# Optimization experiments

Measured on AMD Instinct MI355X. Metric: run time of the kernel, lower is better.

The kernel has to match this reference:

```python
import jax, jax.numpy as jnp
import numpy as np

BATCH = 4096        # config['batch_size']
N_PARTS = 4         # config['n_parts']
TEMP = 0.1          # config['temp_fac']
D = 256             # embedding dim
BS = 3 * BATCH      # bs = 3 * batch_size
EPS = 1e-6          # CosineSimilarity eps


def setup_inputs() -> dict:
    key = jax.random.key(0)
    reg_pred = jax.random.normal(key, (BS, D), dtype=jnp.float32)
    return {"reg_pred": reg_pred}


def reference(reg_pred):
    B, bs, t = BATCH, BS, TEMP
    # cosine similarity: x/max(||x||, eps)
    nrm = jnp.linalg.norm(reg_pred, axis=1, keepdims=True)
    xn = reg_pred / jnp.maximum(nrm, EPS)
    E = jnp.exp((xn @ xn.T) / t)                      # exp(cos_sim/temp), [bs, bs]

    # negative-index mask: for anchor row a (pos_index p = a % B),
    # excluded indices are range(rem, bs, 4) with rem = p % n_parts
    k = jnp.arange(bs)
    rem = (k % B) % N_PARTS                           # rem per anchor row, [bs]
    excluded = (k[None, :] >= rem[:, None]) & (((k[None, :] - rem[:, None]) % 4) == 0)
    den = jnp.sum(jnp.where(excluded, 0.0, E), axis=1)  # [bs], sum exp(den sims)

    p = jnp.arange(B)
    i1, i2, i3 = p, B + p, 2 * B + p

    def pair_loss(a, b, n):
        # symmetrical NT-Xent-style term; n = exp(num_sim / t)
        return -jnp.log(n / (n + den[a])) - jnp.log(n / (n + den[b]))

    n12 = E[i1, i2]
    n13 = E[i1, i3]
    n23 = E[i2, i3]
    total = jnp.sum(pair_loss(i1, i2, n12)
                    + pair_loss(i1, i3, n13)
                    + pair_loss(i2, i3, n23))
    return total / (2 * B)
```

## Files before the change

### kernel.cpp

```cpp
#include <hip/hip_runtime.h>
#include <hip/hip_bf16.h>
#include <cstdint>
#include <cstddef>

#define BS_TOT 12288
#define DIM    256
#define BATCH_ 4096
#define NTILE  96
#define NPAIR  4656

typedef float f32x16 __attribute__((ext_vector_type(16)));
typedef int   i32x8  __attribute__((ext_vector_type(8)));

__global__ __launch_bounds__(256) void normalize_kernel(const float* __restrict__ x,
                                                        uint8_t* __restrict__ xn,
                                                        float* __restrict__ invn,
                                                        float* __restrict__ den,
                                                        float* __restrict__ out,
                                                        int osz) {
  if (blockIdx.x == 0 && (int)threadIdx.x < osz) out[threadIdx.x] = 0.0f;
  const int wave = threadIdx.x >> 6;
  const int lane = threadIdx.x & 63;
  const int row  = blockIdx.x * 4 + wave;
  const float4 v = ((const float4*)(x + (size_t)row * DIM))[lane];
  float ss = v.x*v.x + v.y*v.y + v.z*v.z + v.w*v.w;
  #pragma unroll
  for (int off = 1; off < 64; off <<= 1) ss += __shfl_xor(ss, off, 64);
  const float s = 1.0f / fmaxf(sqrtf(ss), 1e-6f);
  if (lane == 0) { invn[row] = s; den[row] = 0.0f; }
  const float sc = s * 3.79828286f;
  unsigned int w = __builtin_amdgcn_cvt_pk_fp8_f32(v.x * sc, v.y * sc, 0u, false);
  w = __builtin_amdgcn_cvt_pk_fp8_f32(v.z * sc, v.w * sc, w, true);
  ((unsigned int*)(xn + (size_t)row * DIM))[lane] = w;
}

__global__ __launch_bounds__(512, 4) void gemm_den_kernel(const uint8_t* __restrict__ xn,
                                                          float* __restrict__ den) {
  __shared__ __align__(16) uint8_t As[128 * 256];
  __shared__ __align__(16) uint8_t Bs[128 * 256];

  const int tid = threadIdx.x;

  const int t = blockIdx.x;
  int j = (int)((sqrtf(8.0f * (float)t + 1.0f) - 1.0f) * 0.5f);
  while ((j + 1) * (j + 2) / 2 <= t) j++;
  while (j * (j + 1) / 2 > t) j--;
  const int tI = t - j * (j + 1) / 2;
  const int tJ = j;
  const bool offd = (tI != tJ);

  const int wave = tid >> 6, lane = tid & 63;
  const int wr   = wave >> 2;
  const int wc   = wave & 3;
  const int l31  = lane & 31, half = lane >> 5;

  const uint8_t* Ab = xn + (size_t)tI * 128 * DIM;
  const uint8_t* Bb = xn + (size_t)tJ * 128 * DIM;

  int4 chA[4], chB[4];
  #pragma unroll
  for (int c = 0; c < 4; c++) {
    const int q = c * 512 + tid;
    const size_t off = (size_t)(q >> 4) * DIM + (size_t)(q & 15) * 16;
    chA[c] = *(const int4*)(Ab + off);
    chB[c] = *(const int4*)(Bb + off);
  }
  #pragma unroll
  for (int c = 0; c < 4; c++) {
    const int q   = c * 512 + tid;
    const int row = q >> 4, k16 = q & 15;
    const int wa  = row * 256 + (((k16 >> 1) ^ (row & 7)) * 32) + (k16 & 1) * 16;
    *(int4*)(As + wa) = chA[c];
    *(int4*)(Bs + wa) = chB[c];
  }
  __syncthreads();

  const int e7 = l31 & 7;
  const int rowA0 = (wr * 64 + l31) * 256;
  const int rowB0 = (wc * 32 + l31) * 256;

  f32x16 acc[2]  = {};
  f32x16 accT[2] = {};
  #pragma unroll
  for (int ks = 0; ks < 4; ks++) {
    const int u = ((2 * ks + half) ^ e7) * 32;
    i32x8 af[2], bf;
    af[0] = *(const i32x8*)(As + rowA0 + u);
    af[1] = *(const i32x8*)(As + rowA0 + 32 * 256 + u);
    bf    = *(const i32x8*)(Bs + rowB0 + u);
    #pragma unroll
    for (int mi = 0; mi < 2; mi++)
      acc[mi] = __builtin_amdgcn_mfma_scale_f32_32x32x64_f8f6f4(
          af[mi], bf, acc[mi], 0, 0, 0, 0x7F7F7F7F, 0, 0x7F7F7F7F);
    if (offd) {
      #pragma unroll
      for (int mi = 0; mi < 2; mi++)
        accT[mi] = __builtin_amdgcn_mfma_scale_f32_32x32x64_f8f6f4(
            bf, af[mi], accT[mi], 0, 0, 0, 0x7F7F7F7F, 0, 0x7F7F7F7F);
    }
  }

  {
    float cs = 0.0f;
    #pragma unroll
    for (int mi = 0; mi < 2; mi++)
      #pragma unroll
      for (int r = 0; r < 16; r++)
        if (((l31 ^ r) & 3) != 0)
          cs += __builtin_amdgcn_exp2f(acc[mi][r]);
    cs += __shfl_xor(cs, 32, 64);
    if (half == 0) atomicAdd(&den[tJ * 128 + wc * 32 + l31], cs);
  }
  if (offd) {
    #pragma unroll
    for (int mi = 0; mi < 2; mi++) {
      float cs = 0.0f;
      #pragma unroll
      for (int r = 0; r < 16; r++)
        if (((l31 ^ r) & 3) != 0)
          cs += __builtin_amdgcn_exp2f(accT[mi][r]);
      cs += __shfl_xor(cs, 32, 64);
      if (half == 0) atomicAdd(&den[tI * 128 + wr * 64 + mi * 32 + l31], cs);
    }
  }
}

__global__ __launch_bounds__(256) void loss_kernel(const float* __restrict__ x,
                                                   const float* __restrict__ invn,
                                                   const float* __restrict__ den,
                                                   float* __restrict__ out) {
  __shared__ float part[4];
  const int wave = threadIdx.x >> 6, lane = threadIdx.x & 63;
  const int p = blockIdx.x * 4 + wave;
  const float4 a = ((const float4*)(x + (size_t)p * DIM))[lane];
  const float4 b = ((const float4*)(x + (size_t)(BATCH_ + p) * DIM))[lane];
  const float4 c = ((const float4*)(x + (size_t)(2*BATCH_ + p) * DIM))[lane];
  float d12 = a.x*b.x + a.y*b.y + a.z*b.z + a.w*b.w;
  float d13 = a.x*c.x + a.y*c.y + a.z*c.z + a.w*c.w;
  float d23 = b.x*c.x + b.y*c.y + b.z*c.z + b.w*c.w;
  #pragma unroll
  for (int off = 1; off < 64; off <<= 1) {
    d12 += __shfl_xor(d12, off, 64);
    d13 += __shfl_xor(d13, off, 64);
    d23 += __shfl_xor(d23, off, 64);
  }
  if (lane == 0) {
    const float s1 = invn[p], s2 = invn[BATCH_ + p], s3 = invn[2*BATCH_ + p];
    const float z12 = d12 * s1 * s2 * 10.0f;
    const float z13 = d13 * s1 * s3 * 10.0f;
    const float z23 = d23 * s2 * s3 * 10.0f;
    const float n12 = __expf(z12), n13 = __expf(z13), n23 = __expf(z23);
    const float e1 = den[p], e2 = den[BATCH_ + p], e3 = den[2*BATCH_ + p];
    part[wave] = __logf(n12 + e1) + __logf(n12 + e2) - 2.0f * z12
               + __logf(n13 + e1) + __logf(n13 + e3) - 2.0f * z13
               + __logf(n23 + e2) + __logf(n23 + e3) - 2.0f * z23;
  }
  __syncthreads();
  if (threadIdx.x == 0) {
    atomicAdd(out, (part[0] + part[1] + part[2] + part[3]) * (1.0f / (2.0f * BATCH_)));
  }
}

extern "C" void kernel_launch(void* const* d_in, const int* in_sizes, int n_in,
                              void* d_out, int out_size, void* d_ws, size_t ws_size,
                              hipStream_t stream) {
  const float* x = (const float*)d_in[0];
  float* out = (float*)d_out;

  char* ws = (char*)d_ws;
  uint8_t* xn   = (uint8_t*)ws;
  float*   invn = (float*)(ws + (size_t)BS_TOT * DIM);
  float*   den  = (float*)(ws + (size_t)BS_TOT * DIM + BS_TOT * 4);

  normalize_kernel<<<BS_TOT / 4, 256, 0, stream>>>(x, xn, invn, den, out, out_size);
  gemm_den_kernel<<<NPAIR, 512, 0, stream>>>(xn, den);
  loss_kernel<<<BATCH_ / 4, 256, 0, stream>>>(x, invn, den, out);
}
```

Baseline: 124.1 us.

## Make GEMM-den kernel persistent with double-buffered async global-to-LDS loads

Replaces the one-block-per-tile launch with a persistent grid of 256 blocks that stride over the triangular tile pairs. Each block prefetches the next A/B tiles straight into a second LDS buffer with global_load_lds while it computes the current tile, moving the XOR swizzle onto the global-address side. The aim is to hide tile-load latency and cut the cost of launching and scheduling thousands of blocks. In exchange, the doubled LDS footprint allows only one block per CU, and the uneven split of tiles across blocks leaves a small tail.

```diff
diff --git a/kernel.cpp b/kernel.cpp
--- a/kernel.cpp
+++ b/kernel.cpp
@@ -3,14 +3,18 @@
 #include <cstdint>
 #include <cstddef>
 
-#define BS_TOT 12288
-#define DIM    256
-#define BATCH_ 4096
-#define NTILE  96
-#define NPAIR  4656
+#define BS_TOT  12288
+#define DIM     256
+#define BATCH_  4096
+#define NTILE   96
+#define NPAIR   4656
+#define NBLOCKS 256
 
 typedef float f32x16 __attribute__((ext_vector_type(16)));
 typedef int   i32x8  __attribute__((ext_vector_type(8)));
+
+#define AS1 __attribute__((address_space(1)))
+#define AS3 __attribute__((address_space(3)))
 
 __global__ __launch_bounds__(256) void normalize_kernel(const float* __restrict__ x,
                                                         uint8_t* __restrict__ xn,
@@ -34,94 +38,126 @@
   ((unsigned int*)(xn + (size_t)row * DIM))[lane] = w;
 }
 
-__global__ __launch_bounds__(512, 4) void gemm_den_kernel(const uint8_t* __restrict__ xn,
-                                                          float* __restrict__ den) {
-  __shared__ __align__(16) uint8_t As[128 * 256];
-  __shared__ __align__(16) uint8_t Bs[128 * 256];
-
-  const int tid = threadIdx.x;
-
-  const int t = blockIdx.x;
+__device__ __forceinline__ void decode_pair(int t, int& tI, int& tJ) {
   int j = (int)((sqrtf(8.0f * (float)t + 1.0f) - 1.0f) * 0.5f);
   while ((j + 1) * (j + 2) / 2 <= t) j++;
   while (j * (j + 1) / 2 > t) j--;
-  const int tI = t - j * (j + 1) / 2;
-  const int tJ = j;
-  const bool offd = (tI != tJ);
-
+  tI = t - j * (j + 1) / 2;
+  tJ = j;
+}
+
+__global__ __launch_bounds__(512, 2) void gemm_den_kernel(const uint8_t* __restrict__ xn,
+                                                          float* __restrict__ den) {
+  __shared__ __align__(16) uint8_t As[2][128 * 256];
+  __shared__ __align__(16) uint8_t Bs[2][128 * 256];
+
+  const int tid  = threadIdx.x;
   const int wave = tid >> 6, lane = tid & 63;
   const int wr   = wave >> 2;
   const int wc   = wave & 3;
   const int l31  = lane & 31, half = lane >> 5;
-
-  const uint8_t* Ab = xn + (size_t)tI * 128 * DIM;
-  const uint8_t* Bb = xn + (size_t)tJ * 128 * DIM;
-
-  int4 chA[4], chB[4];
-  #pragma unroll
-  for (int c = 0; c < 4; c++) {
-    const int q = c * 512 + tid;
-    const size_t off = (size_t)(q >> 4) * DIM + (size_t)(q & 15) * 16;
-    chA[c] = *(const int4*)(Ab + off);
-    chB[c] = *(const int4*)(Bb + off);
-  }
+  const int e7   = l31 & 7;
+  const int rowA0 = (wr * 64 + l31) * 256;
+  const int rowB0 = (wc * 32 + l31) * 256;
+
+  size_t goff[4]; int loff[4];
   #pragma unroll
   for (int c = 0; c < 4; c++) {
     const int q   = c * 512 + tid;
-    const int row = q >> 4, k16 = q & 15;
-    const int wa  = row * 256 + (((k16 >> 1) ^ (row & 7)) * 32) + (k16 & 1) * 16;
-    *(int4*)(As + wa) = chA[c];
-    *(int4*)(Bs + wa) = chB[c];
-  }
-  __syncthreads();
-
-  const int e7 = l31 & 7;
-  const int rowA0 = (wr * 64 + l31) * 256;
-  const int rowB0 = (wc * 32 + l31) * 256;
-
-  f32x16 acc[2]  = {};
-  f32x16 accT[2] = {};
-  #pragma unroll
-  for (int ks = 0; ks < 4; ks++) {
-    const int u = ((2 * ks + half) ^ e7) * 32;
-    i32x8 af[2], bf;
-    af[0] = *(const i32x8*)(As + rowA0 + u);
-    af[1] = *(const i32x8*)(As + rowA0 + 32 * 256 + u);
-    bf    = *(const i32x8*)(Bs + rowB0 + u);
+    const int row = q >> 4, s = q & 15;
+    const int src16 = (((s >> 1) ^ (row & 7)) * 2) + (s & 1);
+    goff[c] = (size_t)row * DIM + (size_t)src16 * 16;
+    loff[c] = q * 16;
+  }
+
+  int tcur = blockIdx.x;
+  int nI, nJ;
+  decode_pair(tcur, nI, nJ);
+
+  {
+    const uint8_t* Ab = xn + (size_t)nI * 128 * DIM;
+    const uint8_t* Bb = xn + (size_t)nJ * 128 * DIM;
     #pragma unroll
-    for (int mi = 0; mi < 2; mi++)
-      acc[mi] = __builtin_amdgcn_mfma_scale_f32_32x32x64_f8f6f4(
-          af[mi], bf, acc[mi], 0, 0, 0, 0x7F7F7F7F, 0, 0x7F7F7F7F);
+    for (int c = 0; c < 4; c++) {
+      __builtin_amdgcn_global_load_lds((AS1 void*)(Ab + goff[c]),
+                                       (AS3 void*)(&As[0][0] + loff[c]), 16, 0, 0);
+      __builtin_amdgcn_global_load_lds((AS1 void*)(Bb + goff[c]),
+                                       (AS3 void*)(&Bs[0][0] + loff[c]), 16, 0, 0);
+    }
+  }
+  int buf = 0;
+  int curI = nI, curJ = nJ;
+
+  for (;;) {
+    __syncthreads();
+
+    const int  tnext = tcur + NBLOCKS;
+    const bool more  = (tnext < NPAIR);
+    if (more) {
+      decode_pair(tnext, nI, nJ);
+      const uint8_t* An = xn + (size_t)nI * 128 * DIM;
+      const uint8_t* Bn = xn + (size_t)nJ * 128 * DIM;
+      const int nb = buf ^ 1;
+      #pragma unroll
+      for (int c = 0; c < 4; c++) {
+        __builtin_amdgcn_global_load_lds((AS1 void*)(An + goff[c]),
+                                         (AS3 void*)(&As[nb][0] + loff[c]), 16, 0, 0);
+        __builtin_amdgcn_global_load_lds((AS1 void*)(Bn + goff[c]),
+                                         (AS3 void*)(&Bs[nb][0] + loff[c]), 16, 0, 0);
+      }
+    }
+
+    const bool offd = (curI != curJ);
+    const uint8_t* Ac = &As[buf][0];
+    const uint8_t* Bc = &Bs[buf][0];
+
+    f32x16 acc[2]  = {};
+    f32x16 accT[2] = {};
+    #pragma unroll
+    for (int ks = 0; ks < 4; ks++) {
+      const int u = ((2 * ks + half) ^ e7) * 32;
+      i32x8 af[2], bf;
+      af[0] = *(const i32x8*)(Ac + rowA0 + u);
+      af[1] = *(const i32x8*)(Ac + rowA0 + 32 * 256 + u);
+      bf    = *(const i32x8*)(Bc + rowB0 + u);
+      #pragma unroll
+      for (int mi = 0; mi < 2; mi++)
+        acc[mi] = __builtin_amdgcn_mfma_scale_f32_32x32x64_f8f6f4(
+            af[mi], bf, acc[mi], 0, 0, 0, 0x7F7F7F7F, 0, 0x7F7F7F7F);
+      if (offd) {
+        #pragma unroll
+        for (int mi = 0; mi < 2; mi++)
+          accT[mi] = __builtin_amdgcn_mfma_scale_f32_32x32x64_f8f6f4(
+              bf, af[mi], accT[mi], 0, 0, 0, 0x7F7F7F7F, 0, 0x7F7F7F7F);
+      }
+    }
+
+    {
+      float cs = 0.0f;
+      #pragma unroll
+      for (int mi = 0; mi < 2; mi++)
+        #pragma unroll
+        for (int r = 0; r < 16; r++)
+          if (((l31 ^ r) & 3) != 0)
+            cs += __builtin_amdgcn_exp2f(acc[mi][r]);
+      cs += __shfl_xor(cs, 32, 64);
+      if (half == 0) atomicAdd(&den[curJ * 128 + wc * 32 + l31], cs);
+    }
     if (offd) {
       #pragma unroll
-      for (int mi = 0; mi < 2; mi++)
-        accT[mi] = __builtin_amdgcn_mfma_scale_f32_32x32x64_f8f6f4(
-            bf, af[mi], accT[mi], 0, 0, 0, 0x7F7F7F7F, 0, 0x7F7F7F7F);
-    }
-  }
-
-  {
-    float cs = 0.0f;
-    #pragma unroll
-    for (int mi = 0; mi < 2; mi++)
-      #pragma unroll
-      for (int r = 0; r < 16; r++)
-        if (((l31 ^ r) & 3) != 0)
-          cs += __builtin_amdgcn_exp2f(acc[mi][r]);
-    cs += __shfl_xor(cs, 32, 64);
-    if (half == 0) atomicAdd(&den[tJ * 128 + wc * 32 + l31], cs);
-  }
-  if (offd) {
-    #pragma unroll
-    for (int mi = 0; mi < 2; mi++) {
-      float cs = 0.0f;
-      #pragma unroll
-      for (int r = 0; r < 16; r++)
-        if (((l31 ^ r) & 3) != 0)
-          cs += __builtin_amdgcn_exp2f(accT[mi][r]);
-      cs += __shfl_xor(cs, 32, 64);
-      if (half == 0) atomicAdd(&den[tI * 128 + wr * 64 + mi * 32 + l31], cs);
-    }
+      for (int mi = 0; mi < 2; mi++) {
+        float cs = 0.0f;
+        #pragma unroll
+        for (int r = 0; r < 16; r++)
+          if (((l31 ^ r) & 3) != 0)
+            cs += __builtin_amdgcn_exp2f(accT[mi][r]);
+        cs += __shfl_xor(cs, 32, 64);
+        if (half == 0) atomicAdd(&den[curI * 128 + wr * 64 + mi * 32 + l31], cs);
+      }
+    }
+
+    if (!more) break;
+    curI = nI; curJ = nJ; tcur = tnext; buf ^= 1;
   }
 }
 
@@ -173,6 +209,6 @@
   float*   den  = (float*)(ws + (size_t)BS_TOT * DIM + BS_TOT * 4);
 
   normalize_kernel<<<BS_TOT / 4, 256, 0, stream>>>(x, xn, invn, den, out, out_size);
-  gemm_den_kernel<<<NPAIR, 512, 0, stream>>>(xn, den);
+  gemm_den_kernel<<<NBLOCKS, 512, 0, stream>>>(xn, den);
   loss_kernel<<<BATCH_ / 4, 256, 0, stream>>>(x, invn, den, out);
 }
```

After: 134.9 us. 8.7% more time.
